# Performance work log

Hardware: AMD Instinct MI355X
Metric: run time of the kernel (lower is better)

## Reference

```python
import jax, jax.numpy as jnp
import numpy as np

BN_EPS = 1e-5
SCI_NOTATION_THRESHOLD = 1e16  # python float repr uses 'e+' only for |v| >= 1e16
NEG_SLOPE = 0.5


def _rescale(x):
    # Mirrors: str(max_abs.item()).split('e+') -> divide by 10**exponent when repr is scientific.
    m = jnp.max(jnp.abs(x))
    exp = jnp.floor(jnp.log10(jnp.maximum(m, 1.0)))
    return jnp.where(m >= SCI_NOTATION_THRESHOLD, x / (10.0 ** exp), x)


def _block(x, w, b, g, beta):
    # Linear (+ rescale), BatchNorm1d training-mode (+ rescale), LeakyReLU(0.5) (+ rescale)
    x = _rescale(x @ w.T + b)
    mu = jnp.mean(x, axis=0)
    var = jnp.mean(jnp.square(x - mu), axis=0)  # biased var, as torch BN normalization
    x = _rescale(g * (x - mu) * jax.lax.rsqrt(var + BN_EPS) + beta)
    x = _rescale(jnp.where(x >= 0, x, NEG_SLOPE * x))
    return x


def _uniform(k, shape, fan_in):
    bound = 1.0 / np.sqrt(fan_in)
    return jax.random.uniform(k, shape, jnp.float32, -bound, bound)


def setup_inputs() -> dict:
    key = jax.random.key(0)
    ks = jax.random.split(key, 9)
    B, D = 32768, 512
    H1, H2, H3, O = 2048, 2048, 1024, 1
    return {
        "x": jax.random.normal(ks[0], (B, D), jnp.float32),
        "w1": _uniform(ks[1], (H1, D), D),
        "b1": _uniform(ks[2], (H1,), D),
        "g1": jnp.ones((H1,), jnp.float32),
        "be1": jnp.zeros((H1,), jnp.float32),
        "w2": _uniform(ks[3], (H2, H1), H1),
        "b2": _uniform(ks[4], (H2,), H1),
        "g2": jnp.ones((H2,), jnp.float32),
        "be2": jnp.zeros((H2,), jnp.float32),
        "w3": _uniform(ks[5], (H3, H2), H2),
        "b3": _uniform(ks[6], (H3,), H2),
        "g3": jnp.ones((H3,), jnp.float32),
        "be3": jnp.zeros((H3,), jnp.float32),
        "wout": _uniform(ks[7], (O, H3), H3),
        "bout": _uniform(ks[8], (O,), H3),
    }


def reference(x, w1, b1, g1, be1, w2, b2, g2, be2, w3, b3, g3, be3, wout, bout):
    x = _block(x, w1, b1, g1, be1)
    x = _block(x, w2, b2, g2, be2)
    x = _block(x, w3, b3, g3, be3)
    return x @ wout.T + bout  # [B, 1]
```

## Files before the change

### kernel.cpp

```cpp
#include <hip/hip_runtime.h>

typedef __bf16 bf16x8 __attribute__((ext_vector_type(8)));
typedef float f32x4 __attribute__((ext_vector_type(4)));
typedef unsigned short us8 __attribute__((ext_vector_type(8)));

typedef __attribute__((address_space(3))) void lds_void_t;
typedef const __attribute__((address_space(1))) void gbl_void_t;

__device__ __forceinline__ unsigned short f2bf(float f) {
    unsigned u = __builtin_bit_cast(unsigned, f);
    u += 0x7FFFu + ((u >> 16) & 1u);
    return (unsigned short)(u >> 16);
}
__device__ __forceinline__ float bf2f(unsigned short h) {
    unsigned u = ((unsigned)h) << 16;
    return __builtin_bit_cast(float, u);
}

__global__ void report_ws(float* out, float v) { out[0] = v; }

__global__ __launch_bounds__(256) void cast_bf16(
    const float* __restrict__ src, unsigned short* __restrict__ dst, size_t n8)
{
    size_t i = (size_t)blockIdx.x * 256 + threadIdx.x;
    if (i >= n8) return;
    const float4* s = (const float4*)src + i * 2;
    float4 a = s[0], b = s[1];
    us8 o;
    o[0] = f2bf(a.x); o[1] = f2bf(a.y); o[2] = f2bf(a.z); o[3] = f2bf(a.w);
    o[4] = f2bf(b.x); o[5] = f2bf(b.y); o[6] = f2bf(b.z); o[7] = f2bf(b.w);
    *((us8*)dst + i) = o;
}


#define LOAD_AQ(QH) \
  _Pragma("unroll") for (int mm = 0; mm < 4; ++mm) \
    _Pragma("unroll") for (int s = 0; s < 2; ++s) \
      aq[mm][s] = *(const bf16x8*)&lds[aoff + ((QH)*64 + mm*16 + fr)*64 + (((s*4 + fq) ^ w7) << 3)];

#define LOAD_BP(G) \
  _Pragma("unroll") for (int nn = 0; nn < 2; ++nn) \
    _Pragma("unroll") for (int s = 0; s < 2; ++s) \
      bq[(G)*2+nn][s] = *(const bf16x8*)&lds[boff + ((wc&1)*64 + ((G)*2+nn)*16 + fr)*64 + (((s*4 + fq) ^ w7) << 3)];

#define MFMA_QUAD(QH, G) \
  _Pragma("unroll") for (int mm = 0; mm < 4; ++mm) \
    _Pragma("unroll") for (int nn = 0; nn < 2; ++nn) \
      _Pragma("unroll") for (int s = 0; s < 2; ++s) \
        acc[(QH)*4+mm][(G)*2+nn] = __builtin_amdgcn_mfma_f32_16x16x32_bf16( \
            aq[mm][s], bq[(G)*2+nn][s], acc[(QH)*4+mm][(G)*2+nn], 0, 0, 0);

__global__ __launch_bounds__(512, 2) void gemm256(
    const unsigned short* __restrict__ A,
    const unsigned short* __restrict__ W,
    const float* __restrict__ bias,
    unsigned short* __restrict__ Y,
    float* __restrict__ psum, float* __restrict__ psumsq,
    int M, int N, int K, int rowBlkBase)
{
    __shared__ unsigned short lds[65536];

    const int nbx = N >> 8;
    const int nwg = gridDim.x;
    const int cpx = nwg >> 3;
    const int bid = blockIdx.x;
    const int swzb = (bid & 7) * cpx + (bid >> 3);
    const int bm = swzb / nbx;
    const int bn = swzb % nbx;

    const int t    = threadIdx.x;
    const int wid  = t >> 6;
    const int lane = t & 63;
    const int wrh  = wid >> 2;
    const int wc   = wid & 3;
    const int fr   = lane & 15;
    const int fq   = lane >> 4;
    const int w7   = fr & 7;

    const int r0s  = t >> 3;
    const int ce   = (((t & 7) ^ ((t >> 3) & 7)) << 3);

    const size_t baseA = (size_t)(bm << 8) * K;
    const size_t baseW = (size_t)(bn << 8) * K;
    const int NT = K >> 6;

    auto STAGE = [&](int b, int op, int h, int kt) {
        const unsigned short* gsrc = (op ? W : A)
            + (op ? baseW : baseA)
            + (size_t)((h << 7) + r0s) * K + (kt << 6) + ce;
        char* dst = (char*)lds + ((((b * 2 + op) * 2 + h) << 14) + (wid << 10));
        __builtin_amdgcn_global_load_lds((gbl_void_t*)gsrc, (lds_void_t*)dst, 16, 0, 0);
        __builtin_amdgcn_global_load_lds((gbl_void_t*)(gsrc + (size_t)64 * K),
                                         (lds_void_t*)(dst + 8192), 16, 0, 0);
    };

    f32x4 acc[8][4];
#pragma unroll
    for (int m = 0; m < 8; ++m)
#pragma unroll
        for (int n = 0; n < 4; ++n)
            acc[m][n] = (f32x4){0.f, 0.f, 0.f, 0.f};

    STAGE(0, 0, 0, 0); STAGE(0, 0, 1, 0);
    STAGE(0, 1, 0, 0); STAGE(0, 1, 1, 0);
    if (NT > 1) {
        STAGE(1, 0, 0, 1); STAGE(1, 0, 1, 1);
        STAGE(1, 1, 0, 1); STAGE(1, 1, 1, 1);
        asm volatile("s_waitcnt vmcnt(8)" ::: "memory");
    } else {
        asm volatile("s_waitcnt vmcnt(0)" ::: "memory");
    }
    __builtin_amdgcn_s_barrier();

    bf16x8 aq[4][2], bq[4][2];

    for (int kt = 0; kt < NT; ++kt) {
        const int b = kt & 1;
        const unsigned aoff = (unsigned)(b * 4 + wrh) * 8192;
        const unsigned boff = (unsigned)(b * 4 + 2 + (wc >> 1)) * 8192;

        LOAD_AQ(0);
        LOAD_BP(0);
        asm volatile("s_waitcnt lgkmcnt(8)" ::: "memory");
        __builtin_amdgcn_s_barrier();
        asm volatile("s_waitcnt lgkmcnt(0)" ::: "memory");
        __builtin_amdgcn_s_setprio(1);
        MFMA_QUAD(0, 0);
        __builtin_amdgcn_s_setprio(0);
        __builtin_amdgcn_s_barrier();

        LOAD_BP(1);
        __builtin_amdgcn_s_barrier();
        asm volatile("s_waitcnt lgkmcnt(0)" ::: "memory");
        __builtin_amdgcn_s_setprio(1);
        MFMA_QUAD(0, 1);
        __builtin_amdgcn_s_setprio(0);
        __builtin_amdgcn_s_barrier();

        LOAD_AQ(1);
        if (kt + 2 < NT) STAGE(b, 1, 0, kt + 2);
        __builtin_amdgcn_s_barrier();
        asm volatile("s_waitcnt lgkmcnt(0)" ::: "memory");
        __builtin_amdgcn_s_setprio(1);
        MFMA_QUAD(1, 0);
        __builtin_amdgcn_s_setprio(0);
        __builtin_amdgcn_s_barrier();

        if (kt + 2 < NT) {
            STAGE(b, 0, 0, kt + 2);
            STAGE(b, 0, 1, kt + 2);
            STAGE(b, 1, 1, kt + 2);
            asm volatile("s_waitcnt vmcnt(8)" ::: "memory");
        } else {
            asm volatile("s_waitcnt vmcnt(0)" ::: "memory");
        }
        __builtin_amdgcn_s_barrier();
        __builtin_amdgcn_s_setprio(1);
        MFMA_QUAD(1, 1);
        __builtin_amdgcn_s_setprio(0);
        __builtin_amdgcn_s_barrier();
    }

    float bv[4];
#pragma unroll
    for (int nn = 0; nn < 4; ++nn) bv[nn] = bias[(bn << 8) + wc * 64 + nn * 16 + fr];

    float* sSum = (float*)lds;
    float* sSq  = (float*)lds + 256 * 8;
#pragma unroll
    for (int nn = 0; nn < 4; ++nn) {
        float s = 0.f, q = 0.f;
#pragma unroll
        for (int mm = 0; mm < 8; ++mm)
#pragma unroll
            for (int r = 0; r < 4; ++r) {
                float v = acc[mm][nn][r] + bv[nn];
                s += v; q += v * v;
            }
        const int col = wc * 64 + nn * 16 + fr;
        const int sl  = wrh * 4 + fq;
        sSum[col * 8 + sl] = s;
        sSq [col * 8 + sl] = q;
    }
    __syncthreads();
    if (t < 256) {
        float s = 0.f, q = 0.f;
#pragma unroll
        for (int k = 0; k < 8; ++k) { s += sSum[t * 8 + k]; q += sSq[t * 8 + k]; }
        psum  [(size_t)(rowBlkBase + bm) * N + (bn << 8) + t] = s;
        psumsq[(size_t)(rowBlkBase + bm) * N + (bn << 8) + t] = q;
    }
    __syncthreads();

#pragma unroll
    for (int nn = 0; nn < 4; ++nn) {
        const int col = wc * 64 + nn * 16 + fr;
#pragma unroll
        for (int mm = 0; mm < 8; ++mm) {
            const int row0 = wrh * 128 + mm * 16 + fq * 4;
#pragma unroll
            for (int r = 0; r < 4; ++r)
                lds[(row0 + r) * 256 + col] = f2bf(acc[mm][nn][r] + bv[nn]);
        }
    }
    __syncthreads();
    {
        const size_t outBase = (size_t)(bm << 8) * N + (bn << 8);
#pragma unroll
        for (int i = 0; i < 16; ++i) {
            const int u   = t + i * 512;
            const int row = u >> 5, sl = u & 31;
            us8 v = *(const us8*)&lds[row * 256 + sl * 8];
            *(us8*)&Y[outBase + (size_t)row * N + sl * 8] = v;
        }
    }
}

__global__ __launch_bounds__(256) void col_stats2(
    const float* __restrict__ psum, const float* __restrict__ psumsq,
    const float* __restrict__ g, const float* __restrict__ be,
    float* __restrict__ scale, float* __restrict__ shift,
    int N, int NB, float invM)
{
    const int col = blockIdx.x * 256 + threadIdx.x;
    float s = 0.f, ss = 0.f;
    for (int c = 0; c < NB; ++c) {
        s  += psum  [(size_t)c * N + col];
        ss += psumsq[(size_t)c * N + col];
    }
    float mu  = s * invM;
    float var = ss * invM - mu * mu;
    float a = g[col] * rsqrtf(var + 1e-5f);
    scale[col] = a;
    shift[col] = be[col] - mu * a;
}

__global__ __launch_bounds__(256) void norm_full(
    const unsigned short* __restrict__ src, unsigned short* __restrict__ dst,
    const float* __restrict__ scale, const float* __restrict__ shift,
    unsigned colMask8, size_t n8)
{
    const size_t stride = (size_t)gridDim.x * 256;
    for (size_t i = (size_t)blockIdx.x * 256 + threadIdx.x; i < n8; i += stride) {
        us8 v = *((const us8*)src + i);
        const unsigned c8 = (unsigned)i & colMask8;
        const float4* sc = (const float4*)scale + c8 * 2;
        const float4* sh = (const float4*)shift + c8 * 2;
        float4 s0 = sc[0], s1 = sc[1], h0 = sh[0], h1 = sh[1];
        float xs[8];
        xs[0] = bf2f(v[0]) * s0.x + h0.x;  xs[1] = bf2f(v[1]) * s0.y + h0.y;
        xs[2] = bf2f(v[2]) * s0.z + h0.z;  xs[3] = bf2f(v[3]) * s0.w + h0.w;
        xs[4] = bf2f(v[4]) * s1.x + h1.x;  xs[5] = bf2f(v[5]) * s1.y + h1.y;
        xs[6] = bf2f(v[6]) * s1.z + h1.z;  xs[7] = bf2f(v[7]) * s1.w + h1.w;
        us8 o;
#pragma unroll
        for (int j = 0; j < 8; ++j) {
            float x = xs[j];
            x = fmaxf(x, 0.5f * x);
            o[j] = f2bf(x);
        }
        *((us8*)dst + i) = o;
    }
}

__global__ __launch_bounds__(256) void matvec_norm_out(
    const unsigned short* __restrict__ X, const float* __restrict__ scale,
    const float* __restrict__ shift, const float* __restrict__ wvec,
    const float* __restrict__ bout, float* __restrict__ out, int Kd)
{
    const int row  = blockIdx.x * 4 + (threadIdx.x >> 6);
    const int lane = threadIdx.x & 63;
    const unsigned short* xr = X + (size_t)row * Kd;
    float s = 0.f;
    for (int j = lane * 8; j < Kd; j += 512) {
        us8 x = *(const us8*)(xr + j);
        const float4* sc = (const float4*)(scale + j);
        const float4* sh = (const float4*)(shift + j);
        const float4* wv = (const float4*)(wvec + j);
        float4 s0 = sc[0], s1 = sc[1], h0 = sh[0], h1 = sh[1];
        float4 w0 = wv[0], w1 = wv[1];
        float xs[8] = {
            bf2f(x[0]) * s0.x + h0.x, bf2f(x[1]) * s0.y + h0.y,
            bf2f(x[2]) * s0.z + h0.z, bf2f(x[3]) * s0.w + h0.w,
            bf2f(x[4]) * s1.x + h1.x, bf2f(x[5]) * s1.y + h1.y,
            bf2f(x[6]) * s1.z + h1.z, bf2f(x[7]) * s1.w + h1.w };
        float wf[8] = { w0.x, w0.y, w0.z, w0.w, w1.x, w1.y, w1.z, w1.w };
#pragma unroll
        for (int e = 0; e < 8; ++e) {
            float xv = xs[e];
            xv = fmaxf(xv, 0.5f * xv);
            s += xv * wf[e];
        }
    }
#pragma unroll
    for (int off = 32; off > 0; off >>= 1) s += __shfl_down(s, off);
    if (lane == 0) out[row] = s + bout[0];
}

extern "C" void kernel_launch(void* const* d_in, const int* in_sizes, int n_in,
                              void* d_out, int out_size, void* d_ws, size_t ws_size,
                              hipStream_t stream)
{
    const float* x    = (const float*)d_in[0];
    const float* w1   = (const float*)d_in[1];
    const float* b1   = (const float*)d_in[2];
    const float* g1   = (const float*)d_in[3];
    const float* be1  = (const float*)d_in[4];
    const float* w2   = (const float*)d_in[5];
    const float* b2   = (const float*)d_in[6];
    const float* g2   = (const float*)d_in[7];
    const float* be2  = (const float*)d_in[8];
    const float* w3   = (const float*)d_in[9];
    const float* b3   = (const float*)d_in[10];
    const float* g3   = (const float*)d_in[11];
    const float* be3  = (const float*)d_in[12];
    const float* wout = (const float*)d_in[13];
    const float* bout = (const float*)d_in[14];
    float* out = (float*)d_out;

    const int B = 32768, D = 512, H1 = 2048, H2 = 2048, H3 = 1024;
    const int NB = B / 256;
    const int RCH = 16384;
    const float invB = 1.0f / (float)B;
    char* ws = (char*)d_ws;

    size_t off = 0;
    auto alloc = [&](size_t bytes) -> char* {
        char* p = ws + off;
        off += (bytes + 255) & ~(size_t)255;
        return p;
    };
    unsigned short* bufA  = (unsigned short*)alloc((size_t)B * H1 * 2);
    unsigned short* bufY3 = (unsigned short*)alloc((size_t)B * H3 * 2);
    unsigned short* W1b   = (unsigned short*)alloc((size_t)H1 * D * 2);
    unsigned short* W2b   = (unsigned short*)alloc((size_t)H2 * H1 * 2);
    unsigned short* W3b   = (unsigned short*)alloc((size_t)H3 * H2 * 2);
    float* psum   = (float*)alloc((size_t)NB * H1 * 4);
    float* psumsq = (float*)alloc((size_t)NB * H1 * 4);
    float* scale  = (float*)alloc((size_t)H1 * 4);
    float* shift  = (float*)alloc((size_t)H1 * 4);

    if (off > ws_size) {
        report_ws<<<1, 1, 0, stream>>>(out, (float)ws_size);
        return;
    }

    {
        size_t n8;
        n8 = (size_t)B * D / 8;   cast_bf16<<<(unsigned)((n8 + 255) / 256), 256, 0, stream>>>(x,  bufY3, n8);
        n8 = (size_t)H1 * D / 8;  cast_bf16<<<(unsigned)((n8 + 255) / 256), 256, 0, stream>>>(w1, W1b, n8);
        n8 = (size_t)H2 * H1 / 8; cast_bf16<<<(unsigned)((n8 + 255) / 256), 256, 0, stream>>>(w2, W2b, n8);
        n8 = (size_t)H3 * H2 / 8; cast_bf16<<<(unsigned)((n8 + 255) / 256), 256, 0, stream>>>(w3, W3b, n8);
    }

    gemm256<<<(B / 256) * (H1 / 256), 512, 0, stream>>>(
        bufY3, W1b, b1, bufA, psum, psumsq, B, H1, D, 0);
    col_stats2<<<H1 / 256, 256, 0, stream>>>(psum, psumsq, g1, be1, scale, shift, H1, NB, invB);

    const size_t chunk8 = (size_t)RCH * H1 / 8;
    for (int c = 0; c < B / RCH; ++c) {
        norm_full<<<2048, 256, 0, stream>>>(
            bufA + (size_t)c * RCH * H1, bufY3, scale, shift, H1 / 8 - 1, chunk8);
        gemm256<<<(RCH / 256) * (H2 / 256), 512, 0, stream>>>(
            bufY3, W2b, b2, bufA + (size_t)c * RCH * H1, psum, psumsq,
            RCH, H2, H1, c * (RCH / 256));
    }
    col_stats2<<<H2 / 256, 256, 0, stream>>>(psum, psumsq, g2, be2, scale, shift, H2, NB, invB);

    norm_full<<<4096, 256, 0, stream>>>(bufA, bufA, scale, shift, H2 / 8 - 1, (size_t)B * H2 / 8);
    gemm256<<<(B / 256) * (H3 / 256), 512, 0, stream>>>(
        bufA, W3b, b3, bufY3, psum, psumsq, B, H3, H2, 0);
    col_stats2<<<H3 / 256, 256, 0, stream>>>(psum, psumsq, g3, be3, scale, shift, H3, NB, invB);

    matvec_norm_out<<<B / 4, 256, 0, stream>>>(bufY3, scale, shift, wout, bout, out, H3);
}
```

Baseline: 689.3 us.

## Simplify GEMM main loop to one-ahead double buffering with single barrier

Replaces the two-tile-ahead staged prefetch, with its many interleaved barriers and partial vmcnt waits, with a simpler scheme. Each iteration waits for all loads, issues one barrier, then prefetches the whole next tile into the other buffer before running the four MFMA quads without intermediate barriers. This removes many per-iteration barriers and the 8-wave lockstep ping-pong. In exchange it exposes more global-load latency, since prefetch depth drops to one tile and vmcnt(0) stalls every iteration. It also drops the explicit lgkmcnt waits between LDS fragment reads and MFMAs, leaving those to the compiler.

```diff
diff --git a/kernel.cpp b/kernel.cpp
--- a/kernel.cpp
+++ b/kernel.cpp
@@ -103,14 +103,6 @@
 
     STAGE(0, 0, 0, 0); STAGE(0, 0, 1, 0);
     STAGE(0, 1, 0, 0); STAGE(0, 1, 1, 0);
-    if (NT > 1) {
-        STAGE(1, 0, 0, 1); STAGE(1, 0, 1, 1);
-        STAGE(1, 1, 0, 1); STAGE(1, 1, 1, 1);
-        asm volatile("s_waitcnt vmcnt(8)" ::: "memory");
-    } else {
-        asm volatile("s_waitcnt vmcnt(0)" ::: "memory");
-    }
-    __builtin_amdgcn_s_barrier();
 
     bf16x8 aq[4][2], bq[4][2];
 
@@ -119,47 +111,25 @@
         const unsigned aoff = (unsigned)(b * 4 + wrh) * 8192;
         const unsigned boff = (unsigned)(b * 4 + 2 + (wc >> 1)) * 8192;
 
+        asm volatile("s_waitcnt vmcnt(0)" ::: "memory");
+        __builtin_amdgcn_s_barrier();
+        asm volatile("" ::: "memory");
+
+        if (kt + 1 < NT) {
+            STAGE(b ^ 1, 0, 0, kt + 1); STAGE(b ^ 1, 0, 1, kt + 1);
+            STAGE(b ^ 1, 1, 0, kt + 1); STAGE(b ^ 1, 1, 1, kt + 1);
+        }
+
         LOAD_AQ(0);
         LOAD_BP(0);
-        asm volatile("s_waitcnt lgkmcnt(8)" ::: "memory");
-        __builtin_amdgcn_s_barrier();
-        asm volatile("s_waitcnt lgkmcnt(0)" ::: "memory");
-        __builtin_amdgcn_s_setprio(1);
-        MFMA_QUAD(0, 0);
-        __builtin_amdgcn_s_setprio(0);
-        __builtin_amdgcn_s_barrier();
-
+        __builtin_amdgcn_s_setprio(1); MFMA_QUAD(0, 0); __builtin_amdgcn_s_setprio(0);
         LOAD_BP(1);
-        __builtin_amdgcn_s_barrier();
-        asm volatile("s_waitcnt lgkmcnt(0)" ::: "memory");
-        __builtin_amdgcn_s_setprio(1);
-        MFMA_QUAD(0, 1);
-        __builtin_amdgcn_s_setprio(0);
-        __builtin_amdgcn_s_barrier();
-
+        __builtin_amdgcn_s_setprio(1); MFMA_QUAD(0, 1); __builtin_amdgcn_s_setprio(0);
         LOAD_AQ(1);
-        if (kt + 2 < NT) STAGE(b, 1, 0, kt + 2);
-        __builtin_amdgcn_s_barrier();
-        asm volatile("s_waitcnt lgkmcnt(0)" ::: "memory");
-        __builtin_amdgcn_s_setprio(1);
-        MFMA_QUAD(1, 0);
-        __builtin_amdgcn_s_setprio(0);
-        __builtin_amdgcn_s_barrier();
-
-        if (kt + 2 < NT) {
-            STAGE(b, 0, 0, kt + 2);
-            STAGE(b, 0, 1, kt + 2);
-            STAGE(b, 1, 1, kt + 2);
-            asm volatile("s_waitcnt vmcnt(8)" ::: "memory");
-        } else {
-            asm volatile("s_waitcnt vmcnt(0)" ::: "memory");
-        }
-        __builtin_amdgcn_s_barrier();
-        __builtin_amdgcn_s_setprio(1);
-        MFMA_QUAD(1, 1);
-        __builtin_amdgcn_s_setprio(0);
-        __builtin_amdgcn_s_barrier();
-    }
+        __builtin_amdgcn_s_setprio(1); MFMA_QUAD(1, 0); __builtin_amdgcn_s_setprio(0);
+        __builtin_amdgcn_s_setprio(1); MFMA_QUAD(1, 1); __builtin_amdgcn_s_setprio(0);
+    }
+    __syncthreads();
 
     float bv[4];
 #pragma unroll
```

Result: faster. 654.9 us (median of 2 runs) (-5.0%).
